# Kernel optimization log

Measured on AMD Instinct MI355X. Metric: run time of the kernel, lower is better.

## Reference

```python
import jax, jax.numpy as jnp
import numpy as np

N_NODES = 50000
N_EDGES = 800000
N_GRAPHS = 512
NEG_SLOPE = 0.2  # PyG GATConv default LeakyReLU slope


def _gat_layer(x, src, dst, W, a_src, a_dst, b, n_nodes):
    """PyG-style GATConv (concat=True, self-loops already in src/dst)."""
    H, C = a_src.shape
    h = (x @ W).reshape(n_nodes, H, C)            # [N, H, C]
    e_s = (h * a_src).sum(-1)                     # [N, H]
    e_d = (h * a_dst).sum(-1)                     # [N, H]
    e = jax.nn.leaky_relu(e_s[src] + e_d[dst], NEG_SLOPE)  # [E, H]
    # segment softmax over destination nodes
    m = jax.ops.segment_max(e, dst, num_segments=n_nodes)
    w = jnp.exp(e - m[dst])
    s = jax.ops.segment_sum(w, dst, num_segments=n_nodes)
    alpha = w / (s[dst] + 1e-16)                  # [E, H]
    out = jax.ops.segment_sum(h[src] * alpha[:, :, None], dst, num_segments=n_nodes)
    return out.reshape(n_nodes, H * C) + b


def setup_inputs() -> dict:
    key = jax.random.key(0)
    ks = jax.random.split(key, 16)
    x = jax.random.normal(ks[0], (N_NODES, 2), dtype=jnp.float32)
    edge_index = jax.random.randint(ks[1], (2, N_EDGES), 0, N_NODES, dtype=jnp.int64 if jax.config.jax_enable_x64 else jnp.int32)
    batch = jnp.sort(jax.random.randint(ks[2], (N_NODES,), 0, N_GRAPHS))
    g = lambda k, shape: (jax.random.normal(k, shape, dtype=jnp.float32) * 0.1)
    return {
        "x": x, "edge_index": edge_index, "batch": batch,
        "W1": g(ks[3], (2, 64)),   "a1s": g(ks[4], (8, 8)),  "a1d": g(ks[5], (8, 8)),  "b1": jnp.zeros((64,), jnp.float32),
        "W2": g(ks[6], (64, 128)), "a2s": g(ks[7], (8, 16)), "a2d": g(ks[8], (8, 16)), "b2": jnp.zeros((128,), jnp.float32),
        "W3": g(ks[9], (128, 128)),"a3s": g(ks[10], (8, 16)),"a3d": g(ks[11], (8, 16)),"b3": jnp.zeros((128,), jnp.float32),
        "fc1W": g(ks[12], (128, 32)), "fc1b": jnp.zeros((32,), jnp.float32),
        "fc2W": g(ks[13], (32, 10)),  "fc2b": jnp.zeros((10,), jnp.float32),
    }


def reference(x, edge_index, batch, W1, a1s, a1d, b1, W2, a2s, a2d, b2, W3, a3s, a3d, b3, fc1W, fc1b, fc2W, fc2b):
    n = x.shape[0]
    loop = jnp.arange(n, dtype=edge_index.dtype)
    src = jnp.concatenate([edge_index[0], loop])  # add self-loops (PyG default)
    dst = jnp.concatenate([edge_index[1], loop])
    h = jax.nn.elu(_gat_layer(x, src, dst, W1, a1s, a1d, b1, n))
    h = jax.nn.elu(_gat_layer(h, src, dst, W2, a2s, a2d, b2, n))
    h = _gat_layer(h, src, dst, W3, a3s, a3d, b3, n)
    # global mean pool over graphs
    sums = jax.ops.segment_sum(h, batch, num_segments=N_GRAPHS)
    cnt = jax.ops.segment_sum(jnp.ones((n,), h.dtype), batch, num_segments=N_GRAPHS)
    pooled = sums / jnp.maximum(cnt, 1.0)[:, None]   # [G, 128]
    z = jax.nn.relu(pooled @ fc1W + fc1b)
    return jax.nn.log_softmax(z @ fc2W + fc2b, axis=1)
```

## Files before the change

### kernel.cpp

```cpp
#include <hip/hip_runtime.h>
#include <cstddef>
#include <cstdint>


__device__ __forceinline__ unsigned bf16pair(float a, float b) {
    unsigned ua = __float_as_uint(a), ub = __float_as_uint(b);
    ua += 0x7fffu + ((ua >> 16) & 1u);
    ub += 0x7fffu + ((ub >> 16) & 1u);
    return (ua >> 16) | (ub & 0xffff0000u);
}
__device__ __forceinline__ unsigned short bf16one(float a) {
    unsigned ua = __float_as_uint(a);
    ua += 0x7fffu + ((ua >> 16) & 1u);
    return (unsigned short)(ua >> 16);
}


#define BSTRIDE 8192

__global__ __launch_bounds__(256) void bucket1_k(const int* __restrict__ edge,
                                                 unsigned* __restrict__ barr,
                                                 int* __restrict__ bcnt,
                                                 int E, int EA) {
    __shared__ int h[256];
    __shared__ int lbase[256];
    int tid = threadIdx.x;
    h[tid] = 0;
    __syncthreads();
    int start = blockIdx.x * 4096;
    unsigned ent[16];
    int lp[16];
#pragma unroll
    for (int k = 0; k < 16; ++k) {
        int i = start + k * 256 + tid;
        if (i < EA) {
            int s, d;
            if (i < E) { s = edge[i]; d = edge[E + i]; }
            else { s = i - E; d = s; }
            int b = d >> 8;
            ent[k] = (unsigned)s | ((unsigned)(d & 255) << 16) | ((unsigned)b << 24);
            lp[k] = atomicAdd(&h[b], 1);
        } else {
            ent[k] = 0xffffffffu;
            lp[k] = 0;
        }
    }
    __syncthreads();
    lbase[tid] = h[tid] ? atomicAdd(&bcnt[tid], h[tid]) : 0;
    __syncthreads();
#pragma unroll
    for (int k = 0; k < 16; ++k) {
        if (ent[k] != 0xffffffffu) {
            int b = ent[k] >> 24;
            int pos = lbase[b] + lp[k];
            if (pos < BSTRIDE)
                barr[(size_t)b * BSTRIDE + pos] = ent[k] & 0x00ffffffu;
        }
    }
}

__global__ __launch_bounds__(256) void bscan_k(const int* __restrict__ bcnt,
                                               int* __restrict__ bbase,
                                               int* __restrict__ offsets,
                                               int nb, int N, int EA) {
    __shared__ int sd[256];
    int tid = threadIdx.x;
    int v = (tid < nb) ? bcnt[tid] : 0;
    sd[tid] = v;
    __syncthreads();
    for (int off = 1; off < 256; off <<= 1) {
        int t = (tid >= off) ? sd[tid - off] : 0;
        __syncthreads();
        sd[tid] += t;
        __syncthreads();
    }
    if (tid < nb) bbase[tid] = sd[tid] - v;
    if (tid == 0) offsets[N] = EA;
}

__global__ __launch_bounds__(256) void bucket2_k(const unsigned* __restrict__ barr,
                                                 const int* __restrict__ bcnt,
                                                 const int* __restrict__ bbase,
                                                 int* __restrict__ offsets,
                                                 int* __restrict__ esrc, int N) {
    __shared__ int sd[256];
    __shared__ int cur[256];
    int b = blockIdx.x, tid = threadIdx.x;
    int cnt = bcnt[b];
    const unsigned* arr = barr + (size_t)b * BSTRIDE;
    sd[tid] = 0;
    __syncthreads();
    for (int i = tid; i < cnt; i += 256)
        atomicAdd(&sd[(arr[i] >> 16) & 0xff], 1);
    __syncthreads();
    int v = sd[tid];
    for (int off = 1; off < 256; off <<= 1) {
        int t = (tid >= off) ? sd[tid - off] : 0;
        __syncthreads();
        sd[tid] += t;
        __syncthreads();
    }
    int base = bbase[b] + sd[tid] - v;
    int n = b * 256 + tid;
    if (n < N) offsets[n] = base;
    cur[tid] = base;
    __syncthreads();
    for (int i = tid; i < cnt; i += 256) {
        unsigned e = arr[i];
        int pos = atomicAdd(&cur[(e >> 16) & 0xff], 1);
        esrc[pos] = (int)(e & 0xffffu);
    }
}


template <int IN, int NCOL>
__global__ __launch_bounds__(256) void gemm_scores_k(
    const float* __restrict__ x, const float* __restrict__ W,
    const float* __restrict__ a_s, const float* __restrict__ a_d,
    void* __restrict__ h16, float* __restrict__ es, float* __restrict__ ed,
    int n_nodes) {
    constexpr int COLS = NCOL / 64;
    constexpr int CH = (IN < 64) ? IN : 64;
    constexpr int HALVES = (IN + 63) / 64;
    constexpr int K4 = CH / 4;
    __shared__ __align__(16) float Wl[CH * NCOL];
    __shared__ __align__(16) float Xl[32 * CH];
    int wave = threadIdx.x >> 6, lane = threadIdx.x & 63;
    int nbase = blockIdx.x * 32;

    float acc[8][COLS];
#pragma unroll
    for (int it = 0; it < 8; ++it)
#pragma unroll
        for (int c = 0; c < COLS; ++c) acc[it][c] = 0.f;

    for (int hf = 0; hf < HALVES; ++hf) {
        if (hf) __syncthreads();
        for (int i = threadIdx.x; i < CH * NCOL; i += 256)
            Wl[i] = W[hf * 64 * NCOL + i];
        for (int i = threadIdx.x; i < 32 * CH; i += 256) {
            int ln = i / CH, kk = i % CH;
            int n = nbase + ln;
            Xl[i] = (n < n_nodes) ? x[(size_t)n * IN + hf * 64 + kk] : 0.f;
        }
        __syncthreads();

        for (int k4 = 0; k4 < K4; ++k4) {
            float4 xq[8];
#pragma unroll
            for (int it = 0; it < 8; ++it) {
                int ln = it * 4 + wave;
                xq[it] = *(const float4*)&Xl[ln * CH + 4 * k4];
            }
#pragma unroll
            for (int kk = 0; kk < 4; ++kk) {
                int k = 4 * k4 + kk;
                if constexpr (COLS == 2) {
                    float2 wv = ((const float2*)Wl)[k * 64 + lane];
#pragma unroll
                    for (int it = 0; it < 8; ++it) {
                        float xv = ((const float*)&xq[it])[kk];
                        acc[it][0] += xv * wv.x;
                        acc[it][1] += xv * wv.y;
                    }
                } else {
                    float wv = Wl[k * NCOL + lane];
#pragma unroll
                    for (int it = 0; it < 8; ++it) {
                        float xv = ((const float*)&xq[it])[kk];
                        acc[it][0] += xv * wv;
                    }
                }
            }
        }
        for (int k = 4 * K4; k < CH; ++k) {
            if constexpr (COLS == 2) {
                float2 wv = ((const float2*)Wl)[k * 64 + lane];
#pragma unroll
                for (int it = 0; it < 8; ++it) {
                    float xv = Xl[(it * 4 + wave) * CH + k];
                    acc[it][0] += xv * wv.x;
                    acc[it][1] += xv * wv.y;
                }
            } else {
                float wv = Wl[k * NCOL + lane];
#pragma unroll
                for (int it = 0; it < 8; ++it) {
                    float xv = Xl[(it * 4 + wave) * CH + k];
                    acc[it][0] += xv * wv;
                }
            }
        }
    }

    int head = lane >> 3;
#pragma unroll
    for (int it = 0; it < 8; ++it) {
        int n = nbase + it * 4 + wave;
        float ps, pd;
        if constexpr (COLS == 2) {
            int c0 = 2 * lane;
            ps = acc[it][0] * a_s[c0] + acc[it][1] * a_s[c0 + 1];
            pd = acc[it][0] * a_d[c0] + acc[it][1] * a_d[c0 + 1];
        } else {
            ps = acc[it][0] * a_s[lane];
            pd = acc[it][0] * a_d[lane];
        }
#pragma unroll
        for (int off = 1; off < 8; off <<= 1) {
            ps += __shfl_xor(ps, off);
            pd += __shfl_xor(pd, off);
        }
        if (n < n_nodes) {
            if constexpr (COLS == 2) {
                ((unsigned*)h16)[(size_t)n * 64 + lane] =
                    bf16pair(acc[it][0], acc[it][1]);
            } else {
                ((unsigned short*)h16)[(size_t)n * 64 + lane] = bf16one(acc[it][0]);
            }
            if ((lane & 7) == 0) { es[n * 8 + head] = ps; ed[n * 8 + head] = pd; }
        }
    }
}


template <int NCOL, bool ELU>
__global__ __launch_bounds__(256) void gat_k(
    const void* __restrict__ h16, const float* __restrict__ es,
    const float* __restrict__ ed, const int* __restrict__ offsets,
    const int* __restrict__ esrc, const float* __restrict__ bias,
    float* __restrict__ out, int n_nodes) {
    constexpr int UPL = NCOL / 32;
    int wave = threadIdx.x >> 6, lane = threadIdx.x & 63;
    int n = blockIdx.x * 4 + wave;
    if (n >= n_nodes) return;
    int g = lane >> 4;
    int l = lane & 15;
    int head = l >> 1;
    float edn = ed[n * 8 + head];
    int start = offsets[n], end = offsets[n + 1];

    const unsigned* hu = (const unsigned*)h16;
    float acc[2 * UPL];
#pragma unroll
    for (int k = 0; k < 2 * UPL; ++k) acc[k] = 0.f;
    float s = 0.f;

#pragma unroll 2
    for (int j = start; j < end; j += 4) {
        int jj = j + g;
        bool act = (jj < end);
        int src = esrc[act ? jj : end - 1];
        float e0 = es[(size_t)src * 8 + head] + edn;
        float e = fmaxf(e0, 0.2f * e0);
        float p = act ? __expf(e) : 0.f;
        s += p;
        if constexpr (UPL == 4) {
            uint4 u = *(const uint4*)(hu + (size_t)src * 64 + 4 * l);
            acc[0] += p * __uint_as_float(u.x << 16);
            acc[1] += p * __uint_as_float(u.x & 0xffff0000u);
            acc[2] += p * __uint_as_float(u.y << 16);
            acc[3] += p * __uint_as_float(u.y & 0xffff0000u);
            acc[4] += p * __uint_as_float(u.z << 16);
            acc[5] += p * __uint_as_float(u.z & 0xffff0000u);
            acc[6] += p * __uint_as_float(u.w << 16);
            acc[7] += p * __uint_as_float(u.w & 0xffff0000u);
        } else {
            uint2 u = *(const uint2*)(hu + (size_t)src * 32 + 2 * l);
            acc[0] += p * __uint_as_float(u.x << 16);
            acc[1] += p * __uint_as_float(u.x & 0xffff0000u);
            acc[2] += p * __uint_as_float(u.y << 16);
            acc[3] += p * __uint_as_float(u.y & 0xffff0000u);
        }
    }

    s += __shfl_xor(s, 16);
    s += __shfl_xor(s, 32);
#pragma unroll
    for (int k = 0; k < 2 * UPL; ++k) {
        acc[k] += __shfl_xor(acc[k], 16);
        acc[k] += __shfl_xor(acc[k], 32);
    }

    if (g == 0) {
        float r = 1.f / (s + 1e-16f);
        if constexpr (UPL == 4) {
            float4 b0 = ((const float4*)bias)[2 * l];
            float4 b1 = ((const float4*)bias)[2 * l + 1];
            float4 v0, v1;
            v0.x = acc[0] * r + b0.x;  v0.y = acc[1] * r + b0.y;
            v0.z = acc[2] * r + b0.z;  v0.w = acc[3] * r + b0.w;
            v1.x = acc[4] * r + b1.x;  v1.y = acc[5] * r + b1.y;
            v1.z = acc[6] * r + b1.z;  v1.w = acc[7] * r + b1.w;
            if constexpr (ELU) {
                v0.x = (v0.x > 0.f) ? v0.x : expm1f(v0.x);
                v0.y = (v0.y > 0.f) ? v0.y : expm1f(v0.y);
                v0.z = (v0.z > 0.f) ? v0.z : expm1f(v0.z);
                v0.w = (v0.w > 0.f) ? v0.w : expm1f(v0.w);
                v1.x = (v1.x > 0.f) ? v1.x : expm1f(v1.x);
                v1.y = (v1.y > 0.f) ? v1.y : expm1f(v1.y);
                v1.z = (v1.z > 0.f) ? v1.z : expm1f(v1.z);
                v1.w = (v1.w > 0.f) ? v1.w : expm1f(v1.w);
            }
            ((float4*)(out + (size_t)n * 128))[2 * l] = v0;
            ((float4*)(out + (size_t)n * 128))[2 * l + 1] = v1;
        } else {
            float4 b = ((const float4*)bias)[l];
            float4 v;
            v.x = acc[0] * r + b.x;  v.y = acc[1] * r + b.y;
            v.z = acc[2] * r + b.z;  v.w = acc[3] * r + b.w;
            if constexpr (ELU) {
                v.x = (v.x > 0.f) ? v.x : expm1f(v.x);
                v.y = (v.y > 0.f) ? v.y : expm1f(v.y);
                v.z = (v.z > 0.f) ? v.z : expm1f(v.z);
                v.w = (v.w > 0.f) ? v.w : expm1f(v.w);
            }
            ((float4*)(out + (size_t)n * 64))[l] = v;
        }
    }
}


__global__ __launch_bounds__(128) void pool_k(const float* __restrict__ h,
                                              const int* __restrict__ batch,
                                              float* __restrict__ sums,
                                              float* __restrict__ cnt, int n_nodes) {
    int c = threadIdx.x;
    int base = blockIdx.x * 32;
    float acc = 0.f, cacc = 0.f;
    int gprev = -1;
    for (int k = 0; k < 32; k++) {
        int n = base + k;
        if (n >= n_nodes) break;
        int g = batch[n];
        if (g != gprev) {
            if (gprev >= 0) {
                atomicAdd(&sums[gprev * 128 + c], acc);
                if (c == 0) atomicAdd(&cnt[gprev], cacc);
            }
            acc = 0.f; cacc = 0.f; gprev = g;
        }
        acc += h[(size_t)n * 128 + c];
        cacc += 1.f;
    }
    if (gprev >= 0) {
        atomicAdd(&sums[gprev * 128 + c], acc);
        if (c == 0) atomicAdd(&cnt[gprev], cacc);
    }
}


__global__ __launch_bounds__(64) void fc_k(const float* __restrict__ sums,
                                           const float* __restrict__ cnt,
                                           const float* __restrict__ fc1W,
                                           const float* __restrict__ fc1b,
                                           const float* __restrict__ fc2W,
                                           const float* __restrict__ fc2b,
                                           float* __restrict__ out) {
    int g = blockIdx.x, lane = threadIdx.x;
    __shared__ float p[128];
    __shared__ float z[32];
    __shared__ float logits[10];
    float inv = 1.f / fmaxf(cnt[g], 1.f);
    p[lane] = sums[g * 128 + lane] * inv;
    p[lane + 64] = sums[g * 128 + 64 + lane] * inv;
    __syncthreads();
    if (lane < 32) {
        float a = fc1b[lane];
        for (int k = 0; k < 128; k++) a += p[k] * fc1W[k * 32 + lane];
        z[lane] = fmaxf(a, 0.f);
    }
    __syncthreads();
    if (lane < 10) {
        float a = fc2b[lane];
        for (int k = 0; k < 32; k++) a += z[k] * fc2W[k * 10 + lane];
        logits[lane] = a;
    }
    __syncthreads();
    if (lane < 10) {
        float mx = logits[0];
#pragma unroll
        for (int i = 1; i < 10; i++) mx = fmaxf(mx, logits[i]);
        float se = 0.f;
#pragma unroll
        for (int i = 0; i < 10; i++) se += __expf(logits[i] - mx);
        out[g * 10 + lane] = logits[lane] - mx - logf(se);
    }
}


extern "C" void kernel_launch(void* const* d_in, const int* in_sizes, int n_in,
                              void* d_out, int out_size, void* d_ws, size_t ws_size,
                              hipStream_t stream) {
    const float* x = (const float*)d_in[0];
    const int* edge = (const int*)d_in[1];
    const int* batch = (const int*)d_in[2];
    const float* W1 = (const float*)d_in[3];
    const float* a1s = (const float*)d_in[4];
    const float* a1d = (const float*)d_in[5];
    const float* b1 = (const float*)d_in[6];
    const float* W2 = (const float*)d_in[7];
    const float* a2s = (const float*)d_in[8];
    const float* a2d = (const float*)d_in[9];
    const float* b2 = (const float*)d_in[10];
    const float* W3 = (const float*)d_in[11];
    const float* a3s = (const float*)d_in[12];
    const float* a3d = (const float*)d_in[13];
    const float* b3 = (const float*)d_in[14];
    const float* fc1W = (const float*)d_in[15];
    const float* fc1b = (const float*)d_in[16];
    const float* fc2W = (const float*)d_in[17];
    const float* fc2b = (const float*)d_in[18];
    float* out = (float*)d_out;

    const int N = in_sizes[0] / 2;
    const int E = in_sizes[1] / 2;
    const int EA = E + N;
    const int NG = out_size / 10;
    const int NBUCK = (N + 255) >> 8;

    char* p = (char*)d_ws;
    float* hf_a = (float*)p; p += (size_t)N * 128 * 4;
    float* hf_b = (float*)p; p += (size_t)N * 128 * 4;
    unsigned* hb16 = (unsigned*)p; p += (size_t)N * 64 * 4;
    float* es = (float*)p;  p += (size_t)N * 8 * 4;
    float* ed = (float*)p;  p += (size_t)N * 8 * 4;
    float* sums = (float*)p; p += (size_t)NG * 128 * 4;
    float* cnt = (float*)p;  p += (size_t)NG * 4;
    int* bcnt = (int*)p;     p += 256 * 4;
    int* bbase = (int*)p;    p += 256 * 4;
    int* offsets = (int*)p;  p += (size_t)(N + 1) * 4;
    int* esrc = (int*)p;     p += (size_t)(EA + 8) * 4;
    unsigned* barr = (unsigned*)p; p += (size_t)NBUCK * BSTRIDE * 4;

    hipMemsetAsync(sums, 0, ((size_t)NG * 128 + NG + 256) * 4, stream);

    bucket1_k<<<(EA + 4095) / 4096, 256, 0, stream>>>(edge, barr, bcnt, E, EA);
    bscan_k<<<1, 256, 0, stream>>>(bcnt, bbase, offsets, NBUCK, N, EA);
    bucket2_k<<<NBUCK, 256, 0, stream>>>(barr, bcnt, bbase, offsets, esrc, N);

    int gblocks = (N + 31) / 32;
    int ablocks = (N + 3) / 4;
    gemm_scores_k<2, 64><<<gblocks, 256, 0, stream>>>(x, W1, a1s, a1d, hb16, es, ed, N);
    gat_k<64, true><<<ablocks, 256, 0, stream>>>(hb16, es, ed, offsets, esrc, b1, hf_a, N);
    gemm_scores_k<64, 128><<<gblocks, 256, 0, stream>>>(hf_a, W2, a2s, a2d, hb16, es, ed, N);
    gat_k<128, true><<<ablocks, 256, 0, stream>>>(hb16, es, ed, offsets, esrc, b2, hf_b, N);
    gemm_scores_k<128, 128><<<gblocks, 256, 0, stream>>>(hf_b, W3, a3s, a3d, hb16, es, ed, N);
    gat_k<128, false><<<ablocks, 256, 0, stream>>>(hb16, es, ed, offsets, esrc, b3, hf_a, N);

    pool_k<<<(N + 31) / 32, 128, 0, stream>>>(hf_a, batch, sums, cnt, N);
    fc_k<<<NG, 64, 0, stream>>>(sums, cnt, fc1W, fc1b, fc2W, fc2b, out);
}
```

Measured before the change: 324.5 us.

## Use bf16 MFMA GEMMs for layers 2-3 and store intermediate activations in bf16

The dense projections of GAT layers 2 and 3 now run on MFMA 16x16x32 bf16 instructions, using weights pre-shuffled into the MFMA operand layout by a small conversion kernel. The attention score dot products are computed from an LDS-staged output tile. The gat kernels for layers 1 and 2 write bf16 activations instead of fp32, which halves their output traffic and the GEMM input reads. This adds bf16 rounding of the activations that feed the GEMMs, plus two extra small kernel launches.

```diff
diff --git a/kernel.cpp b/kernel.cpp
--- a/kernel.cpp
+++ b/kernel.cpp
@@ -1,6 +1,9 @@
 #include <hip/hip_runtime.h>
 #include <cstddef>
 #include <cstdint>
+
+typedef __attribute__((ext_vector_type(8))) short bf16x8;
+typedef __attribute__((ext_vector_type(4))) float floatx4;
 
 
 __device__ __forceinline__ unsigned bf16pair(float a, float b) {
@@ -113,6 +116,17 @@
 }
 
 
+__global__ void wconv_k(const float* __restrict__ W,
+                        unsigned short* __restrict__ Wt, int total) {
+    int o = blockIdx.x * 256 + threadIdx.x;
+    if (o >= total) return;
+    int j = o & 7, lane = (o >> 3) & 63, ct = (o >> 9) & 7, ks = o >> 12;
+    int k = ks * 32 + (lane >> 4) * 8 + j;
+    int n = ct * 16 + (lane & 15);
+    Wt[o] = bf16one(W[k * 128 + n]);
+}
+
+
 template <int IN, int NCOL>
 __global__ __launch_bounds__(256) void gemm_scores_k(
     const float* __restrict__ x, const float* __restrict__ W,
@@ -121,8 +135,6 @@
     int n_nodes) {
     constexpr int COLS = NCOL / 64;
     constexpr int CH = (IN < 64) ? IN : 64;
-    constexpr int HALVES = (IN + 63) / 64;
-    constexpr int K4 = CH / 4;
     __shared__ __align__(16) float Wl[CH * NCOL];
     __shared__ __align__(16) float Xl[32 * CH];
     int wave = threadIdx.x >> 6, lane = threadIdx.x & 63;
@@ -134,61 +146,30 @@
 #pragma unroll
         for (int c = 0; c < COLS; ++c) acc[it][c] = 0.f;
 
-    for (int hf = 0; hf < HALVES; ++hf) {
-        if (hf) __syncthreads();
-        for (int i = threadIdx.x; i < CH * NCOL; i += 256)
-            Wl[i] = W[hf * 64 * NCOL + i];
-        for (int i = threadIdx.x; i < 32 * CH; i += 256) {
-            int ln = i / CH, kk = i % CH;
-            int n = nbase + ln;
-            Xl[i] = (n < n_nodes) ? x[(size_t)n * IN + hf * 64 + kk] : 0.f;
-        }
-        __syncthreads();
-
-        for (int k4 = 0; k4 < K4; ++k4) {
-            float4 xq[8];
+    for (int i = threadIdx.x; i < CH * NCOL; i += 256)
+        Wl[i] = W[i];
+    for (int i = threadIdx.x; i < 32 * CH; i += 256) {
+        int ln = i / CH, kk = i % CH;
+        int n = nbase + ln;
+        Xl[i] = (n < n_nodes) ? x[(size_t)n * IN + kk] : 0.f;
+    }
+    __syncthreads();
+
+    for (int k = 0; k < CH; ++k) {
+        if constexpr (COLS == 2) {
+            float2 wv = ((const float2*)Wl)[k * 64 + lane];
 #pragma unroll
             for (int it = 0; it < 8; ++it) {
-                int ln = it * 4 + wave;
-                xq[it] = *(const float4*)&Xl[ln * CH + 4 * k4];
+                float xv = Xl[(it * 4 + wave) * CH + k];
+                acc[it][0] += xv * wv.x;
+                acc[it][1] += xv * wv.y;
             }
-#pragma unroll
-            for (int kk = 0; kk < 4; ++kk) {
-                int k = 4 * k4 + kk;
-                if constexpr (COLS == 2) {
-                    float2 wv = ((const float2*)Wl)[k * 64 + lane];
-#pragma unroll
-                    for (int it = 0; it < 8; ++it) {
-                        float xv = ((const float*)&xq[it])[kk];
-                        acc[it][0] += xv * wv.x;
-                        acc[it][1] += xv * wv.y;
-                    }
-                } else {
-                    float wv = Wl[k * NCOL + lane];
-#pragma unroll
-                    for (int it = 0; it < 8; ++it) {
-                        float xv = ((const float*)&xq[it])[kk];
-                        acc[it][0] += xv * wv;
-                    }
-                }
-            }
-        }
-        for (int k = 4 * K4; k < CH; ++k) {
-            if constexpr (COLS == 2) {
-                float2 wv = ((const float2*)Wl)[k * 64 + lane];
-#pragma unroll
-                for (int it = 0; it < 8; ++it) {
-                    float xv = Xl[(it * 4 + wave) * CH + k];
-                    acc[it][0] += xv * wv.x;
-                    acc[it][1] += xv * wv.y;
-                }
-            } else {
-                float wv = Wl[k * NCOL + lane];
-#pragma unroll
-                for (int it = 0; it < 8; ++it) {
-                    float xv = Xl[(it * 4 + wave) * CH + k];
-                    acc[it][0] += xv * wv;
-                }
+        } else {
+            float wv = Wl[k * NCOL + lane];
+#pragma unroll
+            for (int it = 0; it < 8; ++it) {
+                float xv = Xl[(it * 4 + wave) * CH + k];
+                acc[it][0] += xv * wv;
             }
         }
     }
@@ -224,12 +205,85 @@
 }
 
 
-template <int NCOL, bool ELU>
+template <int IN>
+__global__ __launch_bounds__(256) void gemm_mfma_k(
+    const unsigned short* __restrict__ a16, const unsigned short* __restrict__ Wt,
+    const float* __restrict__ a_s, const float* __restrict__ a_d,
+    unsigned* __restrict__ h16, float* __restrict__ es, float* __restrict__ ed,
+    int n_nodes) {
+    constexpr int KSTEPS = IN / 32;
+    __shared__ float Cl[64 * 132];
+    int wave = threadIdx.x >> 6, lane = threadIdx.x & 63;
+    int q = lane >> 4, m = lane & 15;
+    int rbase = blockIdx.x * 64;
+
+    floatx4 acc[8];
+#pragma unroll
+    for (int ct = 0; ct < 8; ++ct) acc[ct] = (floatx4){0.f, 0.f, 0.f, 0.f};
+
+    int ra = rbase + wave * 16 + m;
+    if (ra >= n_nodes) ra = n_nodes - 1;
+    const unsigned short* arow = a16 + (size_t)ra * IN + q * 8;
+
+#pragma unroll
+    for (int ks = 0; ks < KSTEPS; ++ks) {
+        bf16x8 af = *(const bf16x8*)(arow + ks * 32);
+        const unsigned short* wp = Wt + ((size_t)(ks * 8) * 64 + lane) * 8;
+#pragma unroll
+        for (int ct = 0; ct < 8; ++ct) {
+            bf16x8 bf = *(const bf16x8*)(wp + (size_t)ct * 64 * 8);
+            acc[ct] = __builtin_amdgcn_mfma_f32_16x16x32_bf16(af, bf, acc[ct], 0, 0, 0);
+        }
+    }
+
+#pragma unroll
+    for (int ct = 0; ct < 8; ++ct)
+#pragma unroll
+        for (int i = 0; i < 4; ++i)
+            Cl[(wave * 16 + q * 4 + i) * 132 + ct * 16 + m] = acc[ct][i];
+    __syncthreads();
+
+    int rl = threadIdx.x >> 2, part = threadIdx.x & 3;
+    int r = rbase + rl;
+    if (r < n_nodes) {
+        const float* cp = &Cl[rl * 132 + part * 32];
+        float e0s = 0.f, e0d = 0.f, e1s = 0.f, e1d = 0.f;
+#pragma unroll
+        for (int c = 0; c < 16; ++c) {
+            float v = cp[c];
+            int ai = part * 32 + c;
+            e0s += v * a_s[ai];
+            e0d += v * a_d[ai];
+        }
+#pragma unroll
+        for (int c = 16; c < 32; ++c) {
+            float v = cp[c];
+            int ai = part * 32 + c;
+            e1s += v * a_s[ai];
+            e1d += v * a_d[ai];
+        }
+        unsigned pk[16];
+#pragma unroll
+        for (int u = 0; u < 16; ++u) pk[u] = bf16pair(cp[2 * u], cp[2 * u + 1]);
+        uint4* hp = (uint4*)(h16 + (size_t)r * 64) + part * 4;
+        hp[0] = make_uint4(pk[0], pk[1], pk[2], pk[3]);
+        hp[1] = make_uint4(pk[4], pk[5], pk[6], pk[7]);
+        hp[2] = make_uint4(pk[8], pk[9], pk[10], pk[11]);
+        hp[3] = make_uint4(pk[12], pk[13], pk[14], pk[15]);
+        es[r * 8 + 2 * part] = e0s;
+        es[r * 8 + 2 * part + 1] = e1s;
+        ed[r * 8 + 2 * part] = e0d;
+        ed[r * 8 + 2 * part + 1] = e1d;
+    }
+}
+
+
+template <int NCOL, bool ELU, bool OUT16>
 __global__ __launch_bounds__(256) void gat_k(
     const void* __restrict__ h16, const float* __restrict__ es,
     const float* __restrict__ ed, const int* __restrict__ offsets,
     const int* __restrict__ esrc, const float* __restrict__ bias,
-    float* __restrict__ out, int n_nodes) {
+    void* __restrict__ outp, int n_nodes) {
     constexpr int UPL = NCOL / 32;
     int wave = threadIdx.x >> 6, lane = threadIdx.x & 63;
     int n = blockIdx.x * 4 + wave;
@@ -284,38 +338,39 @@
 
     if (g == 0) {
         float r = 1.f / (s + 1e-16f);
-        if constexpr (UPL == 4) {
-            float4 b0 = ((const float4*)bias)[2 * l];
-            float4 b1 = ((const float4*)bias)[2 * l + 1];
-            float4 v0, v1;
-            v0.x = acc[0] * r + b0.x;  v0.y = acc[1] * r + b0.y;
-            v0.z = acc[2] * r + b0.z;  v0.w = acc[3] * r + b0.w;
-            v1.x = acc[4] * r + b1.x;  v1.y = acc[5] * r + b1.y;
-            v1.z = acc[6] * r + b1.z;  v1.w = acc[7] * r + b1.w;
-            if constexpr (ELU) {
-                v0.x = (v0.x > 0.f) ? v0.x : expm1f(v0.x);
-                v0.y = (v0.y > 0.f) ? v0.y : expm1f(v0.y);
-                v0.z = (v0.z > 0.f) ? v0.z : expm1f(v0.z);
-                v0.w = (v0.w > 0.f) ? v0.w : expm1f(v0.w);
-                v1.x = (v1.x > 0.f) ? v1.x : expm1f(v1.x);
-                v1.y = (v1.y > 0.f) ? v1.y : expm1f(v1.y);
-                v1.z = (v1.z > 0.f) ? v1.z : expm1f(v1.z);
-                v1.w = (v1.w > 0.f) ? v1.w : expm1f(v1.w);
+        float v[2 * UPL];
+#pragma unroll
+        for (int k = 0; k < 2 * UPL; ++k) {
+            float b = bias[(2 * UPL) * l + k];
+            float t = acc[k] * r + b;
+            if constexpr (ELU) t = (t > 0.f) ? t : expm1f(t);
+            v[k] = t;
+        }
+        if constexpr (OUT16) {
+            if constexpr (UPL == 4) {
+                uint4 pk;
+                pk.x = bf16pair(v[0], v[1]);
+                pk.y = bf16pair(v[2], v[3]);
+                pk.z = bf16pair(v[4], v[5]);
+                pk.w = bf16pair(v[6], v[7]);
+                ((uint4*)outp)[(size_t)n * 16 + l] = pk;
+            } else {
+                uint2 pk;
+                pk.x = bf16pair(v[0], v[1]);
+                pk.y = bf16pair(v[2], v[3]);
+                ((uint2*)outp)[(size_t)n * 16 + l] = pk;
             }
-            ((float4*)(out + (size_t)n * 128))[2 * l] = v0;
-            ((float4*)(out + (size_t)n * 128))[2 * l + 1] = v1;
         } else {
-            float4 b = ((const float4*)bias)[l];
-            float4 v;
-            v.x = acc[0] * r + b.x;  v.y = acc[1] * r + b.y;
-            v.z = acc[2] * r + b.z;  v.w = acc[3] * r + b.w;
-            if constexpr (ELU) {
-                v.x = (v.x > 0.f) ? v.x : expm1f(v.x);
-                v.y = (v.y > 0.f) ? v.y : expm1f(v.y);
-                v.z = (v.z > 0.f) ? v.z : expm1f(v.z);
-                v.w = (v.w > 0.f) ? v.w : expm1f(v.w);
+            float* out = (float*)outp;
+            if constexpr (UPL == 4) {
+                ((float4*)(out + (size_t)n * 128))[2 * l] =
+                    make_float4(v[0], v[1], v[2], v[3]);
+                ((float4*)(out + (size_t)n * 128))[2 * l + 1] =
+                    make_float4(v[4], v[5], v[6], v[7]);
+            } else {
+                ((float4*)(out + (size_t)n * 64))[l] =
+                    make_float4(v[0], v[1], v[2], v[3]);
             }
-            ((float4*)(out + (size_t)n * 64))[l] = v;
         }
     }
 }
@@ -421,8 +476,11 @@
 
     char* p = (char*)d_ws;
     float* hf_a = (float*)p; p += (size_t)N * 128 * 4;
-    float* hf_b = (float*)p; p += (size_t)N * 128 * 4;
     unsigned* hb16 = (unsigned*)p; p += (size_t)N * 64 * 4;
+    unsigned short* a16a = (unsigned short*)p; p += (size_t)N * 64 * 2;
+    unsigned short* a16b = (unsigned short*)p; p += (size_t)N * 128 * 2;
+    unsigned short* Wt2 = (unsigned short*)p; p += (size_t)64 * 128 * 2;
+    unsigned short* Wt3 = (unsigned short*)p; p += (size_t)128 * 128 * 2;
     float* es = (float*)p;  p += (size_t)N * 8 * 4;
     float* ed = (float*)p;  p += (size_t)N * 8 * 4;
     float* sums = (float*)p; p += (size_t)NG * 128 * 4;
@@ -438,15 +496,18 @@
     bucket1_k<<<(EA + 4095) / 4096, 256, 0, stream>>>(edge, barr, bcnt, E, EA);
     bscan_k<<<1, 256, 0, stream>>>(bcnt, bbase, offsets, NBUCK, N, EA);
     bucket2_k<<<NBUCK, 256, 0, stream>>>(barr, bcnt, bbase, offsets, esrc, N);
+    wconv_k<<<(64 * 128 + 255) / 256, 256, 0, stream>>>(W2, Wt2, 64 * 128);
+    wconv_k<<<(128 * 128 + 255) / 256, 256, 0, stream>>>(W3, Wt3, 128 * 128);
 
     int gblocks = (N + 31) / 32;
+    int mblocks = (N + 63) / 64;
     int ablocks = (N + 3) / 4;
     gemm_scores_k<2, 64><<<gblocks, 256, 0, stream>>>(x, W1, a1s, a1d, hb16, es, ed, N);
-    gat_k<64, true><<<ablocks, 256, 0, stream>>>(hb16, es, ed, offsets, esrc, b1, hf_a, N);
-    gemm_scores_k<64, 128><<<gblocks, 256, 0, stream>>>(hf_a, W2, a2s, a2d, hb16, es, ed, N);
-    gat_k<128, true><<<ablocks, 256, 0, stream>>>(hb16, es, ed, offsets, esrc, b2, hf_b, N);
-    gemm_scores_k<128, 128><<<gblocks, 256, 0, stream>>>(hf_b, W3, a3s, a3d, hb16, es, ed, N);
-    gat_k<128, false><<<ablocks, 256, 0, stream>>>(hb16, es, ed, offsets, esrc, b3, hf_a, N);
+    gat_k<64, true, true><<<ablocks, 256, 0, stream>>>(hb16, es, ed, offsets, esrc, b1, a16a, N);
+    gemm_mfma_k<64><<<mblocks, 256, 0, stream>>>(a16a, Wt2, a2s, a2d, hb16, es, ed, N);
+    gat_k<128, true, true><<<ablocks, 256, 0, stream>>>(hb16, es, ed, offsets, esrc, b2, a16b, N);
+    gemm_mfma_k<128><<<mblocks, 256, 0, stream>>>(a16b, Wt3, a3s, a3d, hb16, es, ed, N);
+    gat_k<128, false, false><<<ablocks, 256, 0, stream>>>(hb16, es, ed, offsets, esrc, b3, hf_a, N);
 
     pool_k<<<(N + 31) / 32, 128, 0, stream>>>(hf_a, batch, sums, cnt, N);
     fc_k<<<NG, 64, 0, stream>>>(sums, cnt, fc1W, fc1b, fc2W, fc2b, out);
```

After: 318.1 us. 1.02x faster.
